# Performance work log

Measured on AMD Instinct MI355X. Metric: run time of the kernel, lower is better.

## Reference

```python
import jax, jax.numpy as jnp
import numpy as np

N, NODE_IN, EDGE_IN, H, ROUNDS = 768, 64, 32, 128, 2


def setup_inputs() -> dict:
    key = jax.random.key(0)
    ks = jax.random.split(key, 12)
    node_feats = jax.random.normal(ks[0], (N, NODE_IN), dtype=jnp.float32)
    edge_feats = jax.random.normal(ks[1], (N, N, EDGE_IN), dtype=jnp.float32)
    adj_mask = jax.random.randint(ks[2], (N, N), 0, 2).astype(jnp.float32)
    def lin(k, fan_in, fan_out):
        w = jax.random.normal(k, (fan_in, fan_out), dtype=jnp.float32) / jnp.sqrt(fan_in)
        return w
    return {
        "node_feats": node_feats,
        "edge_feats": edge_feats,
        "adj_mask": adj_mask,
        "Wn": lin(ks[3], NODE_IN, H), "bn": jnp.zeros((H,), jnp.float32),
        "We": lin(ks[4], EDGE_IN, H), "be": jnp.zeros((H,), jnp.float32),
        "Wa": lin(ks[5], 2 * H, H), "ba": jnp.zeros((H,), jnp.float32),
        "Wu": lin(ks[6], 2 * H, H), "bu": jnp.zeros((H,), jnp.float32),
    }


def reference(node_feats, edge_feats, adj_mask, Wn, bn, We, be, Wa, ba, Wu, bu):
    relu = jax.nn.relu
    h = relu(node_feats @ Wn + bn)                      # (N, H)
    e = relu(jnp.einsum('ijf,fk->ijk', edge_feats, We) + be)  # (N, N, H)
    deg = jnp.clip(adj_mask.sum(axis=0), 1.0)[:, None]  # (N, 1) receiver degree
    # Precompute edge contribution to agg_lin once (constant across rounds):
    # concat([sender, e]) @ Wa == sender @ Wa[:H] + e @ Wa[H:]
    e_proj = jnp.einsum('ijh,hk->ijk', e, Wa[H:])       # (N, N, H)
    for _ in range(ROUNDS):
        s_proj = h @ Wa[:H]                              # (N, H) sender part
        msgs = relu(s_proj[:, None, :] + e_proj + ba)    # (N, N, H)
        agg = jnp.einsum('ijk,ij->jk', msgs, adj_mask) / deg  # masked sum over senders i
        h = relu(jnp.concatenate([h, agg], axis=-1) @ Wu + bu)
    graph_emb = h.mean(axis=0)
    return (h, graph_emb)
```

## Files before the change

### kernel.cpp

```cpp
#include <hip/hip_runtime.h>
#include <hip/hip_bf16.h>


typedef __bf16 bf16x8 __attribute__((ext_vector_type(8)));
typedef float f32x4 __attribute__((ext_vector_type(4)));

#define NN 768

static __device__ __forceinline__ unsigned short to_bf16u(float x) {
    return __builtin_bit_cast(unsigned short, (__bf16)x);
}

__global__ __launch_bounds__(256) void k_prep(
                       const float* __restrict__ adj,
                       const float* __restrict__ We, const float* __restrict__ Wa,
                       unsigned short* __restrict__ WeT, unsigned short* __restrict__ Wa2T,
                       const float* __restrict__ nf, const float* __restrict__ Wn,
                       const float* __restrict__ bn, const float* __restrict__ ba,
                       float* __restrict__ h, float* __restrict__ sp,
                       float* __restrict__ invdeg) {
    const int b = blockIdx.x, tid = threadIdx.x;
    if (b < 80) {
        int g = b * 256 + tid;
        if (g < 128 * 32) {
            int c = g >> 5, f = g & 31;
            WeT[g] = to_bf16u(We[f * 128 + c]);
        } else {
            int g2 = g - 128 * 32;
            int c = g2 >> 7, k = g2 & 127;
            Wa2T[g2] = to_bf16u(Wa[(128 + k) * 128 + c]);
        }
    } else if (b < 464) {
        __shared__ float nf_l[2][64];
        __shared__ float h_l[2][128];
        int row = tid >> 7, t = tid & 127;
        int i = (b - 80) * 2 + row;
        if (t < 64) nf_l[row][t] = nf[i * 64 + t];
        __syncthreads();
        float acc = bn[t];
#pragma unroll 8
        for (int f = 0; f < 64; ++f) acc += nf_l[row][f] * Wn[f * 128 + t];
        acc = fmaxf(acc, 0.f);
        h[i * 128 + t] = acc;
        h_l[row][t] = acc;
        __syncthreads();
        float spv = ba[t];
#pragma unroll 8
        for (int f = 0; f < 128; ++f) spv += h_l[row][f] * Wa[f * 128 + t];
        sp[i * 128 + t] = spv;
    } else {
        __shared__ float dsum[4][64];
        int d = b - 464;
        int q = tid >> 6, jj = tid & 63;
        int j = d * 64 + jj;
        float s = 0.f;
        for (int i = q * 192; i < q * 192 + 192; ++i)
            s += adj[(size_t)i * NN + j];
        dsum[q][jj] = s;
        __syncthreads();
        if (tid < 64) {
            float tot = dsum[0][tid] + dsum[1][tid] + dsum[2][tid] + dsum[3][tid];
            invdeg[d * 64 + tid] = 1.0f / fmaxf(tot, 1.0f);
        }
    }
}

__global__ __launch_bounds__(512) void k_build(
    const float* __restrict__ ef, const unsigned short* __restrict__ WeT,
    const unsigned short* __restrict__ Wa2T, const float* __restrict__ be,
    unsigned short* __restrict__ eproj) {
    __shared__ __align__(16) unsigned short e_lds[2][32 * 128];
    __shared__ __align__(16) unsigned short o_lds[2][32 * 128];
    const int tid  = threadIdx.x;
    const int lane = tid & 63;
    const int wv   = tid >> 6;
    const int wr   = wv >> 2;
    const int wc   = wv & 3;
    const int lg   = lane >> 4;
    const int lr   = lane & 15;
    const size_t gbase = (size_t)blockIdx.x * NN;

    bf16x8 bwe[2];
    bf16x8 bwa[2][4];
    f32x4 bev[2];
#pragma unroll
    for (int t = 0; t < 2; ++t) {
        const int col = 32 * wc + 16 * t + lr;
        bwe[t] = *reinterpret_cast<const bf16x8*>(WeT + col * 32 + 8 * lg);
        bev[t] = *reinterpret_cast<const f32x4*>(be + 32 * wc + 16 * t + 4 * lg);
#pragma unroll
        for (int s = 0; s < 4; ++s)
            bwa[t][s] = *reinterpret_cast<const bf16x8*>(Wa2T + col * 128 + 32 * s + 8 * lg);
    }

    auto load_a = [&](int n, bf16x8& x) {
        const float* p = ef + (gbase + 32 * n + 16 * wr + lr) * 32 + 8 * lg;
        float4 f0 = *reinterpret_cast<const float4*>(p);
        float4 f1 = *reinterpret_cast<const float4*>(p + 4);
        x[0] = (__bf16)f0.x; x[1] = (__bf16)f0.y; x[2] = (__bf16)f0.z; x[3] = (__bf16)f0.w;
        x[4] = (__bf16)f1.x; x[5] = (__bf16)f1.y; x[6] = (__bf16)f1.z; x[7] = (__bf16)f1.w;
    };
    auto gemm1 = [&](bf16x8 aef, int buf) {
        const int row = 16 * wr + lr;
#pragma unroll
        for (int t = 0; t < 2; ++t) {
            f32x4 D = __builtin_amdgcn_mfma_f32_16x16x32_bf16(bwe[t], aef, bev[t], 0, 0, 0);
            ushort4 pk;
            pk.x = to_bf16u(fmaxf(D[0], 0.f));
            pk.y = to_bf16u(fmaxf(D[1], 0.f));
            pk.z = to_bf16u(fmaxf(D[2], 0.f));
            pk.w = to_bf16u(fmaxf(D[3], 0.f));
            int cb = 32 * wc + 16 * t + 4 * lg;
            int idx = (row * 128 + cb) ^ ((row & 7) << 3);
            *reinterpret_cast<ushort4*>(&e_lds[buf][idx]) = pk;
        }
    };

    bf16x8 cA, pA;
    load_a(0, cA);
    gemm1(cA, 0);
    load_a(1, cA);
    __syncthreads();

    for (int n = 0; n < 24; ++n) {
        const int b = n & 1;
        if (n + 2 < 24) load_a(n + 2, pA);
        if (n + 1 < 24) gemm1(cA, b ^ 1);

        const int row = 16 * wr + lr;
        bf16x8 eb[4];
#pragma unroll
        for (int s = 0; s < 4; ++s) {
            int idx = (row * 128 + 32 * s + 8 * lg) ^ ((row & 7) << 3);
            eb[s] = *reinterpret_cast<const bf16x8*>(&e_lds[b][idx]);
        }
#pragma unroll
        for (int t = 0; t < 2; ++t) {
            f32x4 D;
            D[0] = 0.f; D[1] = 0.f; D[2] = 0.f; D[3] = 0.f;
#pragma unroll
            for (int s = 0; s < 4; ++s)
                D = __builtin_amdgcn_mfma_f32_16x16x32_bf16(bwa[t][s], eb[s], D, 0, 0, 0);
            ushort4 pk;
            pk.x = to_bf16u(D[0]); pk.y = to_bf16u(D[1]);
            pk.z = to_bf16u(D[2]); pk.w = to_bf16u(D[3]);
            int cb = 32 * wc + 16 * t + 4 * lg;
            int idx = (row * 128 + cb) ^ ((row & 7) << 3);
            *reinterpret_cast<ushort4*>(&o_lds[b][idx]) = pk;
        }
        __syncthreads();

        {
            const int srow = tid >> 4, a = tid & 15;
            int idx = srow * 128 + 8 * (a ^ (srow & 7));
            f32x4 v = *reinterpret_cast<const f32x4*>(&o_lds[b][idx]);
            *reinterpret_cast<f32x4*>(eproj + (gbase + 32 * n + srow) * 128 + 8 * a) = v;
        }

        if (n + 2 < 24) cA = pA;
    }
}

__global__ __launch_bounds__(256) void k_round(
    const unsigned short* __restrict__ eproj, const float* __restrict__ adj,
    const float* __restrict__ sp, float* __restrict__ aggp) {
    const int tid = threadIdx.x;
    const int jt  = blockIdx.x >> 4;
    const int seg = blockIdx.x & 15;
    const int j0  = jt * 16;
    const int i0  = seg * 48;
    const int jj  = tid >> 4;
    const int kb  = (tid & 15) * 8;

    const size_t estep = (size_t)NN * 128;
    const unsigned short* ep = eproj + ((size_t)i0 * NN + j0 + jj) * 128 + kb;
    const float* ap = adj + (size_t)i0 * NN + j0 + jj;
    const float* spp = sp + (size_t)i0 * 128 + kb;

    float acc[8] = {0.f, 0.f, 0.f, 0.f, 0.f, 0.f, 0.f, 0.f};

    bf16x8 v = *reinterpret_cast<const bf16x8*>(ep);
    float av = *ap;
    float4 s0 = *reinterpret_cast<const float4*>(spp);
    float4 s1 = *reinterpret_cast<const float4*>(spp + 4);

    for (int m = 0; m < 48; ++m) {
        bf16x8 vn = v; float avn = av; float4 s0n = s0, s1n = s1;
        if (m < 47) {
            vn = *reinterpret_cast<const bf16x8*>(ep + estep);
            avn = ap[NN];
            s0n = *reinterpret_cast<const float4*>(spp + 128);
            s1n = *reinterpret_cast<const float4*>(spp + 132);
        }
        acc[0] += fmaxf(s0.x + (float)v[0], 0.f) * av;
        acc[1] += fmaxf(s0.y + (float)v[1], 0.f) * av;
        acc[2] += fmaxf(s0.z + (float)v[2], 0.f) * av;
        acc[3] += fmaxf(s0.w + (float)v[3], 0.f) * av;
        acc[4] += fmaxf(s1.x + (float)v[4], 0.f) * av;
        acc[5] += fmaxf(s1.y + (float)v[5], 0.f) * av;
        acc[6] += fmaxf(s1.z + (float)v[6], 0.f) * av;
        acc[7] += fmaxf(s1.w + (float)v[7], 0.f) * av;
        ep += estep; ap += NN; spp += 128;
        v = vn; av = avn; s0 = s0n; s1 = s1n;
    }

    float* dst = aggp + ((size_t)(j0 + jj) * 16 + seg) * 128 + kb;
    float4 o0, o1;
    o0.x = acc[0]; o0.y = acc[1]; o0.z = acc[2]; o0.w = acc[3];
    o1.x = acc[4]; o1.y = acc[5]; o1.z = acc[6]; o1.w = acc[7];
    *reinterpret_cast<float4*>(dst) = o0;
    *reinterpret_cast<float4*>(dst + 4) = o1;
}

template <int LAST>
__global__ __launch_bounds__(256) void k_upd(
                      const float* __restrict__ h_in, const float* __restrict__ aggp,
                      const float* __restrict__ invdeg,
                      const float* __restrict__ Wu, const float* __restrict__ bu,
                      const float* __restrict__ Wa, const float* __restrict__ ba,
                      float* __restrict__ h_out, float* __restrict__ sp,
                      float* __restrict__ out) {
    __shared__ float buf[2][256];
    __shared__ float hn[2][128];
    const int tid = threadIdx.x;
    const int row = tid >> 7, t = tid & 127;
    const int j = blockIdx.x * 2 + row;
    float s = 0.f;
#pragma unroll
    for (int seg = 0; seg < 16; ++seg)
        s += aggp[((size_t)j * 16 + seg) * 128 + t];
    buf[row][t] = h_in[j * 128 + t];
    buf[row][128 + t] = s * invdeg[j];
    __syncthreads();
    float acc = bu[t];
#pragma unroll 8
    for (int f = 0; f < 256; ++f) acc += buf[row][f] * Wu[f * 128 + t];
    acc = fmaxf(acc, 0.f);
    if (LAST) {
        out[j * 128 + t] = acc;
    } else {
        h_out[j * 128 + t] = acc;
        hn[row][t] = acc;
        __syncthreads();
        float spv = ba[t];
#pragma unroll 8
        for (int f = 0; f < 128; ++f) spv += hn[row][f] * Wa[f * 128 + t];
        sp[j * 128 + t] = spv;
    }
}

__global__ __launch_bounds__(64) void k_gemb(const float* __restrict__ out_h, float* __restrict__ out) {
    int c = blockIdx.x, l = threadIdx.x;
    float acc = 0.f;
    for (int i = l; i < NN; i += 64) acc += out_h[(size_t)i * 128 + c];
#pragma unroll
    for (int off = 32; off; off >>= 1) acc += __shfl_down(acc, off);
    if (l == 0) out[NN * 128 + c] = acc * (1.0f / 768.0f);
}

extern "C" void kernel_launch(void* const* d_in, const int* in_sizes, int n_in,
                              void* d_out, int out_size, void* d_ws, size_t ws_size,
                              hipStream_t stream) {
    const float* nf  = (const float*)d_in[0];
    const float* ef  = (const float*)d_in[1];
    const float* adj = (const float*)d_in[2];
    const float* Wn  = (const float*)d_in[3];
    const float* bn  = (const float*)d_in[4];
    const float* We  = (const float*)d_in[5];
    const float* be  = (const float*)d_in[6];
    const float* Wa  = (const float*)d_in[7];
    const float* ba  = (const float*)d_in[8];
    const float* Wu  = (const float*)d_in[9];
    const float* bu  = (const float*)d_in[10];
    float* out = (float*)d_out;

    float* h_buf  = (float*)d_ws;
    float* sp     = h_buf + NN * 128;
    float* invdeg = sp + NN * 128;
    float* aggp   = invdeg + NN;
    unsigned short* WeT   = (unsigned short*)(aggp + (size_t)NN * 16 * 128);
    unsigned short* Wa2T  = WeT + 128 * 32;
    unsigned short* eproj = Wa2T + 128 * 128;

    k_prep<<<476, 256, 0, stream>>>(adj, We, Wa, WeT, Wa2T, nf, Wn, bn, ba,
                                    h_buf, sp, invdeg);
    k_build<<<NN, 512, 0, stream>>>(ef, WeT, Wa2T, be, eproj);

    k_round<<<48 * 16, 256, 0, stream>>>(eproj, adj, sp, aggp);
    k_upd<0><<<NN / 2, 256, 0, stream>>>(h_buf, aggp, invdeg, Wu, bu, Wa, ba, h_buf, sp, out);
    k_round<<<48 * 16, 256, 0, stream>>>(eproj, adj, sp, aggp);
    k_upd<1><<<NN / 2, 256, 0, stream>>>(h_buf, aggp, invdeg, Wu, bu, Wa, ba, h_buf, sp, out);

    k_gemb<<<128, 64, 0, stream>>>(out, out);
}
```

Before: 142.6 us.

## Fuse edge-projection build with first message-passing round

```diff
diff --git a/kernel.cpp b/kernel.cpp
--- a/kernel.cpp
+++ b/kernel.cpp
@@ -65,100 +65,101 @@
     }
 }
 
-__global__ __launch_bounds__(512) void k_build(
-    const float* __restrict__ ef, const unsigned short* __restrict__ WeT,
+__global__ __launch_bounds__(512) void k_bfr(
+    const float* __restrict__ ef, const float* __restrict__ adj,
+    const float* __restrict__ sp, const unsigned short* __restrict__ WeT,
     const unsigned short* __restrict__ Wa2T, const float* __restrict__ be,
-    unsigned short* __restrict__ eproj) {
-    __shared__ __align__(16) unsigned short e_lds[2][32 * 128];
-    __shared__ __align__(16) unsigned short o_lds[2][32 * 128];
+    unsigned short* __restrict__ eproj, float* __restrict__ aggp) {
+    __shared__ __align__(16) unsigned short e_lds[2][16 * 128];
+    __shared__ __align__(16) unsigned short o_lds[2][16 * 128];
     const int tid  = threadIdx.x;
     const int lane = tid & 63;
     const int wv   = tid >> 6;
-    const int wr   = wv >> 2;
-    const int wc   = wv & 3;
     const int lg   = lane >> 4;
     const int lr   = lane & 15;
-    const size_t gbase = (size_t)blockIdx.x * NN;
-
-    bf16x8 bwe[2];
-    bf16x8 bwa[2][4];
-    f32x4 bev[2];
-#pragma unroll
-    for (int t = 0; t < 2; ++t) {
-        const int col = 32 * wc + 16 * t + lr;
-        bwe[t] = *reinterpret_cast<const bf16x8*>(WeT + col * 32 + 8 * lg);
-        bev[t] = *reinterpret_cast<const f32x4*>(be + 32 * wc + 16 * t + 4 * lg);
-#pragma unroll
-        for (int s = 0; s < 4; ++s)
-            bwa[t][s] = *reinterpret_cast<const bf16x8*>(Wa2T + col * 128 + 32 * s + 8 * lg);
-    }
-
-    auto load_a = [&](int n, bf16x8& x) {
-        const float* p = ef + (gbase + 32 * n + 16 * wr + lr) * 32 + 8 * lg;
+    const int jt   = blockIdx.x >> 4;
+    const int iseg = blockIdx.x & 15;
+    const int j0   = jt * 16;
+    const int ibase = iseg * 48;
+
+    const int col = 16 * wv + lr;
+    bf16x8 bwe = *reinterpret_cast<const bf16x8*>(WeT + col * 32 + 8 * lg);
+    f32x4  bev = *reinterpret_cast<const f32x4*>(be + 16 * wv + 4 * lg);
+    bf16x8 bwa[4];
+#pragma unroll
+    for (int s = 0; s < 4; ++s)
+        bwa[s] = *reinterpret_cast<const bf16x8*>(Wa2T + col * 128 + 32 * s + 8 * lg);
+
+    auto load_a = [&](int ii, bf16x8& x) {
+        const float* p = ef + ((size_t)ii * NN + j0 + lr) * 32 + 8 * lg;
         float4 f0 = *reinterpret_cast<const float4*>(p);
         float4 f1 = *reinterpret_cast<const float4*>(p + 4);
         x[0] = (__bf16)f0.x; x[1] = (__bf16)f0.y; x[2] = (__bf16)f0.z; x[3] = (__bf16)f0.w;
         x[4] = (__bf16)f1.x; x[5] = (__bf16)f1.y; x[6] = (__bf16)f1.z; x[7] = (__bf16)f1.w;
     };
     auto gemm1 = [&](bf16x8 aef, int buf) {
-        const int row = 16 * wr + lr;
-#pragma unroll
-        for (int t = 0; t < 2; ++t) {
-            f32x4 D = __builtin_amdgcn_mfma_f32_16x16x32_bf16(bwe[t], aef, bev[t], 0, 0, 0);
-            ushort4 pk;
-            pk.x = to_bf16u(fmaxf(D[0], 0.f));
-            pk.y = to_bf16u(fmaxf(D[1], 0.f));
-            pk.z = to_bf16u(fmaxf(D[2], 0.f));
-            pk.w = to_bf16u(fmaxf(D[3], 0.f));
-            int cb = 32 * wc + 16 * t + 4 * lg;
-            int idx = (row * 128 + cb) ^ ((row & 7) << 3);
-            *reinterpret_cast<ushort4*>(&e_lds[buf][idx]) = pk;
-        }
+        f32x4 D = __builtin_amdgcn_mfma_f32_16x16x32_bf16(bwe, aef, bev, 0, 0, 0);
+        ushort4 pk;
+        pk.x = to_bf16u(fmaxf(D[0], 0.f));
+        pk.y = to_bf16u(fmaxf(D[1], 0.f));
+        pk.z = to_bf16u(fmaxf(D[2], 0.f));
+        pk.w = to_bf16u(fmaxf(D[3], 0.f));
+        int idx = (lr * 128 + 16 * wv + 4 * lg) ^ ((lr & 7) << 3);
+        *reinterpret_cast<ushort4*>(&e_lds[buf][idx]) = pk;
     };
 
+    f32x4 acc;
+    acc[0] = 0.f; acc[1] = 0.f; acc[2] = 0.f; acc[3] = 0.f;
+
     bf16x8 cA, pA;
-    load_a(0, cA);
+    load_a(ibase, cA);
     gemm1(cA, 0);
-    load_a(1, cA);
+    load_a(ibase + 1, cA);
     __syncthreads();
 
-    for (int n = 0; n < 24; ++n) {
-        const int b = n & 1;
-        if (n + 2 < 24) load_a(n + 2, pA);
-        if (n + 1 < 24) gemm1(cA, b ^ 1);
-
-        const int row = 16 * wr + lr;
+    for (int m = 0; m < 48; ++m) {
+        const int b = m & 1;
+        const int ii = ibase + m;
+        if (m + 2 < 48) load_a(ibase + m + 2, pA);
+        if (m + 1 < 48) gemm1(cA, b ^ 1);
+
         bf16x8 eb[4];
 #pragma unroll
         for (int s = 0; s < 4; ++s) {
-            int idx = (row * 128 + 32 * s + 8 * lg) ^ ((row & 7) << 3);
+            int idx = (lr * 128 + 32 * s + 8 * lg) ^ ((lr & 7) << 3);
             eb[s] = *reinterpret_cast<const bf16x8*>(&e_lds[b][idx]);
         }
-#pragma unroll
-        for (int t = 0; t < 2; ++t) {
-            f32x4 D;
-            D[0] = 0.f; D[1] = 0.f; D[2] = 0.f; D[3] = 0.f;
-#pragma unroll
-            for (int s = 0; s < 4; ++s)
-                D = __builtin_amdgcn_mfma_f32_16x16x32_bf16(bwa[t][s], eb[s], D, 0, 0, 0);
-            ushort4 pk;
-            pk.x = to_bf16u(D[0]); pk.y = to_bf16u(D[1]);
-            pk.z = to_bf16u(D[2]); pk.w = to_bf16u(D[3]);
-            int cb = 32 * wc + 16 * t + 4 * lg;
-            int idx = (row * 128 + cb) ^ ((row & 7) << 3);
-            *reinterpret_cast<ushort4*>(&o_lds[b][idx]) = pk;
-        }
-        __syncthreads();
-
-        {
+        f32x4 D;
+        D[0] = 0.f; D[1] = 0.f; D[2] = 0.f; D[3] = 0.f;
+#pragma unroll
+        for (int s = 0; s < 4; ++s)
+            D = __builtin_amdgcn_mfma_f32_16x16x32_bf16(bwa[s], eb[s], D, 0, 0, 0);
+
+        f32x4 spv = *reinterpret_cast<const f32x4*>(sp + (size_t)ii * 128 + 16 * wv + 4 * lg);
+        float av = adj[(size_t)ii * NN + j0 + lr];
+#pragma unroll
+        for (int r = 0; r < 4; ++r)
+            acc[r] += fmaxf(D[r] + spv[r], 0.f) * av;
+
+        ushort4 pk;
+        pk.x = to_bf16u(D[0]); pk.y = to_bf16u(D[1]);
+        pk.z = to_bf16u(D[2]); pk.w = to_bf16u(D[3]);
+        int oidx = (lr * 128 + 16 * wv + 4 * lg) ^ ((lr & 7) << 3);
+        *reinterpret_cast<ushort4*>(&o_lds[b][oidx]) = pk;
+        __syncthreads();
+
+        if (tid < 256) {
             const int srow = tid >> 4, a = tid & 15;
             int idx = srow * 128 + 8 * (a ^ (srow & 7));
             f32x4 v = *reinterpret_cast<const f32x4*>(&o_lds[b][idx]);
-            *reinterpret_cast<f32x4*>(eproj + (gbase + 32 * n + srow) * 128 + 8 * a) = v;
-        }
-
-        if (n + 2 < 24) cA = pA;
-    }
+            *reinterpret_cast<f32x4*>(eproj + ((size_t)ii * NN + j0 + srow) * 128 + 8 * a) = v;
+        }
+
+        if (m + 2 < 48) cA = pA;
+    }
+
+    *reinterpret_cast<f32x4*>(
+        aggp + ((size_t)(j0 + lr) * 16 + iseg) * 128 + 16 * wv + 4 * lg) = acc;
 }
 
 __global__ __launch_bounds__(256) void k_round(
@@ -284,10 +285,10 @@
 
     k_prep<<<476, 256, 0, stream>>>(adj, We, Wa, WeT, Wa2T, nf, Wn, bn, ba,
                                     h_buf, sp, invdeg);
-    k_build<<<NN, 512, 0, stream>>>(ef, WeT, Wa2T, be, eproj);
-
-    k_round<<<48 * 16, 256, 0, stream>>>(eproj, adj, sp, aggp);
+
+    k_bfr<<<48 * 16, 512, 0, stream>>>(ef, adj, sp, WeT, Wa2T, be, eproj, aggp);
     k_upd<0><<<NN / 2, 256, 0, stream>>>(h_buf, aggp, invdeg, Wu, bu, Wa, ba, h_buf, sp, out);
+
     k_round<<<48 * 16, 256, 0, stream>>>(eproj, adj, sp, aggp);
     k_upd<1><<<NN / 2, 256, 0, stream>>>(h_buf, aggp, invdeg, Wu, bu, Wa, ba, h_buf, sp, out);
 
```

Measured after the change: 155.8 us. 1.09x slower.
